# Kernel optimization log

Measured on AMD Instinct MI355X. Metric: run time of the kernel, lower is better.

The kernel has to match this reference:

```python
import jax, jax.numpy as jnp
import numpy as np

B, S, I, H, O = 4096, 512, 1, 16, 1


def setup_inputs() -> dict:
    key = jax.random.key(0)
    ks = jax.random.split(key, 7)
    bound = 1.0 / np.sqrt(H)
    return {
        "x": jax.random.normal(ks[0], (B, S, I), dtype=jnp.float32),
        "W_ih": jax.random.uniform(ks[1], (H, I), minval=-bound, maxval=bound, dtype=jnp.float32),
        "W_hh": jax.random.uniform(ks[2], (H, H), minval=-bound, maxval=bound, dtype=jnp.float32),
        "b_ih": jax.random.uniform(ks[3], (H,), minval=-bound, maxval=bound, dtype=jnp.float32),
        "b_hh": jax.random.uniform(ks[4], (H,), minval=-bound, maxval=bound, dtype=jnp.float32),
        "W_fc": jax.random.uniform(ks[5], (O, H), minval=-bound, maxval=bound, dtype=jnp.float32),
        "b_fc": jax.random.uniform(ks[6], (O,), minval=-bound, maxval=bound, dtype=jnp.float32),
    }


def reference(x, W_ih, W_hh, b_ih, b_hh, W_fc, b_fc):
    # Vanilla RNN (tanh): h_t = tanh(x_t W_ih^T + b_ih + h_{t-1} W_hh^T + b_hh)
    # Precompute input projections for all timesteps in one GEMM: [B,S,H]
    x_proj = jnp.einsum('bsi,hi->bsh', x, W_ih) + b_ih + b_hh

    def step(h, xp_t):  # h: [B,H], xp_t: [B,H]
        h_new = jnp.tanh(xp_t + h @ W_hh.T)
        return h_new, None

    h0 = jnp.zeros((x.shape[0], W_hh.shape[0]), dtype=x.dtype)
    h_last, _ = jax.lax.scan(step, h0, jnp.swapaxes(x_proj, 0, 1))  # scan over S
    # out[:, -1, :] -> final linear
    return h_last @ W_fc.T + b_fc
```

## Files before the change

### kernel.cpp

```cpp
#include <hip/hip_runtime.h>


#define S2LE 2.8853900817779268f

#define ROTI(v, N) __builtin_amdgcn_mov_dpp((v), 0x120 + (N), 0xF, 0xF, 0)
#define ROTF(v, N) __int_as_float(__builtin_amdgcn_mov_dpp(__float_as_int(v), 0x120 + (N), 0xF, 0xF, 0))

__global__ __launch_bounds__(64) void rnn_kernel(
    const float* __restrict__ x,
    const float* __restrict__ W_ih,
    const float* __restrict__ W_hh,
    const float* __restrict__ b_ih,
    const float* __restrict__ b_hh,
    const float* __restrict__ W_fc,
    const float* __restrict__ b_fc,
    float* __restrict__ out)
{
    const int li = (int)(threadIdx.x & 15u);
    const int b  = (int)((blockIdx.x * 64u + threadIdx.x) >> 4);

    const float* __restrict__ row = W_hh + li * 16;

    float w[16];
    w[0] = row[li] * S2LE;
#define LW(N) { int s_ = ROTI(li, N); w[N] = row[s_] * S2LE; }
    LW(1) LW(2) LW(3) LW(4) LW(5) LW(6) LW(7) LW(8)
    LW(9) LW(10) LW(11) LW(12) LW(13) LW(14) LW(15)
#undef LW

    const float wih  = W_ih[li] * S2LE;
    const float bias = (b_ih[li] + b_hh[li]) * S2LE;
    const float wfc  = W_fc[li];
    const float bfc  = b_fc[0];

    const float4* __restrict__ xv = (const float4*)(x + (size_t)b * 512);

    float h = 0.0f;
    float4 xc = xv[0];

#define STEP(XV) do { \
    float y0 = fmaf((XV), wih, bias); \
    y0 = fmaf(w[0], h, y0); \
    y0 = fmaf(w[1], ROTF(h, 1), y0); \
    y0 = fmaf(w[2], ROTF(h, 2), y0); \
    y0 = fmaf(w[3], ROTF(h, 3), y0); \
    float y1 = w[4] * ROTF(h, 4); \
    y1 = fmaf(w[5], ROTF(h, 5), y1); \
    y1 = fmaf(w[6], ROTF(h, 6), y1); \
    y1 = fmaf(w[7], ROTF(h, 7), y1); \
    float y2 = w[8] * ROTF(h, 8); \
    y2 = fmaf(w[9], ROTF(h, 9), y2); \
    y2 = fmaf(w[10], ROTF(h, 10), y2); \
    y2 = fmaf(w[11], ROTF(h, 11), y2); \
    float y3 = w[12] * ROTF(h, 12); \
    y3 = fmaf(w[13], ROTF(h, 13), y3); \
    y3 = fmaf(w[14], ROTF(h, 14), y3); \
    y3 = fmaf(w[15], ROTF(h, 15), y3); \
    y0 = (y0 + y1) + (y2 + y3); \
    float e_ = __builtin_amdgcn_exp2f(y0); \
    float r_ = __builtin_amdgcn_rcpf(e_ + 1.0f); \
    h = fmaf(-2.0f, r_, 1.0f); \
} while (0)

#pragma unroll 1
    for (int c = 0; c < 128; ++c) {
        float4 xn = xv[(c + 1) & 127];
        STEP(xc.x);
        STEP(xc.y);
        STEP(xc.z);
        STEP(xc.w);
        xc = xn;
    }
#undef STEP

    float p = h * wfc;
    p += ROTF(p, 8);
    p += ROTF(p, 4);
    p += ROTF(p, 2);
    p += ROTF(p, 1);
    if (li == 0) out[b] = p + bfc;
}

extern "C" void kernel_launch(void* const* d_in, const int* in_sizes, int n_in,
                              void* d_out, int out_size, void* d_ws, size_t ws_size,
                              hipStream_t stream) {
    const float* x    = (const float*)d_in[0];
    const float* W_ih = (const float*)d_in[1];
    const float* W_hh = (const float*)d_in[2];
    const float* b_ih = (const float*)d_in[3];
    const float* b_hh = (const float*)d_in[4];
    const float* W_fc = (const float*)d_in[5];
    const float* b_fc = (const float*)d_in[6];
    float* out = (float*)d_out;

    rnn_kernel<<<1024, 64, 0, stream>>>(x, W_ih, W_hh, b_ih, b_hh, W_fc, b_fc, out);
}
```

Before: 109.9 us.

## Compute RNN recurrence with fp16 MFMA on sigmoid-reparameterized hidden state

Replaces the per-lane DPP-rotate FMA chain with a 16x16x16 f16 MFMA per timestep. Each wave now handles 16 batch rows instead of 4, so the grid shrinks from 1024 to 256 blocks. The hidden state is rewritten as h = 1 - 2*sigmoid, with the row-sum of W_hh folded into the bias and -2 folded into the weights, which turns each step into one MFMA plus four exp/rcp per lane. The cost is fp16 precision for the weights and hidden state across 512 dependent steps, plus fewer waves to hide MFMA and transcendental latency.

```diff
diff --git a/kernel.cpp b/kernel.cpp
--- a/kernel.cpp
+++ b/kernel.cpp
@@ -3,8 +3,8 @@
 
 #define S2LE 2.8853900817779268f
 
-#define ROTI(v, N) __builtin_amdgcn_mov_dpp((v), 0x120 + (N), 0xF, 0xF, 0)
-#define ROTF(v, N) __int_as_float(__builtin_amdgcn_mov_dpp(__float_as_int(v), 0x120 + (N), 0xF, 0xF, 0))
+typedef _Float16 half4 __attribute__((ext_vector_type(4)));
+typedef float float4_ __attribute__((ext_vector_type(4)));
 
 __global__ __launch_bounds__(64) void rnn_kernel(
     const float* __restrict__ x,
@@ -16,69 +16,74 @@
     const float* __restrict__ b_fc,
     float* __restrict__ out)
 {
-    const int li = (int)(threadIdx.x & 15u);
-    const int b  = (int)((blockIdx.x * 64u + threadIdx.x) >> 4);
+    const int l  = (int)threadIdx.x;
+    const int n  = l & 15;
+    const int q  = l >> 4;
+    const int bb = (int)blockIdx.x * 16;
 
-    const float* __restrict__ row = W_hh + li * 16;
+    half4 afrag;
+#pragma unroll
+    for (int i = 0; i < 4; ++i)
+        afrag[i] = (_Float16)(-2.0f * S2LE * W_hh[n * 16 + (4 * q + i)]);
 
-    float w[16];
-    w[0] = row[li] * S2LE;
-#define LW(N) { int s_ = ROTI(li, N); w[N] = row[s_] * S2LE; }
-    LW(1) LW(2) LW(3) LW(4) LW(5) LW(6) LW(7) LW(8)
-    LW(9) LW(10) LW(11) LW(12) LW(13) LW(14) LW(15)
-#undef LW
+    float wih[4], bias[4], wfc[4];
+#pragma unroll
+    for (int r = 0; r < 4; ++r) {
+        int i = 4 * q + r;
+        float sw = 0.0f;
+#pragma unroll
+        for (int j = 0; j < 16; ++j) sw += W_hh[i * 16 + j];
+        wih[r]  = W_ih[i] * S2LE;
+        bias[r] = (b_ih[i] + b_hh[i] + sw) * S2LE;
+        wfc[r]  = W_fc[i];
+    }
 
-    const float wih  = W_ih[li] * S2LE;
-    const float bias = (b_ih[li] + b_hh[li]) * S2LE;
-    const float wfc  = W_fc[li];
-    const float bfc  = b_fc[0];
+    const float4_* __restrict__ xv =
+        (const float4_*)(x + (size_t)(bb + n) * 512);
 
-    const float4* __restrict__ xv = (const float4*)(x + (size_t)b * 512);
+    half4 bfrag;
+    bfrag[0] = bfrag[1] = bfrag[2] = bfrag[3] = (_Float16)0.5f;
+    float4_ gs;
 
-    float h = 0.0f;
-    float4 xc = xv[0];
+    float4_ xc = xv[0];
+    float4_ xn = xv[1];
 
-#define STEP(XV) do { \
-    float y0 = fmaf((XV), wih, bias); \
-    y0 = fmaf(w[0], h, y0); \
-    y0 = fmaf(w[1], ROTF(h, 1), y0); \
-    y0 = fmaf(w[2], ROTF(h, 2), y0); \
-    y0 = fmaf(w[3], ROTF(h, 3), y0); \
-    float y1 = w[4] * ROTF(h, 4); \
-    y1 = fmaf(w[5], ROTF(h, 5), y1); \
-    y1 = fmaf(w[6], ROTF(h, 6), y1); \
-    y1 = fmaf(w[7], ROTF(h, 7), y1); \
-    float y2 = w[8] * ROTF(h, 8); \
-    y2 = fmaf(w[9], ROTF(h, 9), y2); \
-    y2 = fmaf(w[10], ROTF(h, 10), y2); \
-    y2 = fmaf(w[11], ROTF(h, 11), y2); \
-    float y3 = w[12] * ROTF(h, 12); \
-    y3 = fmaf(w[13], ROTF(h, 13), y3); \
-    y3 = fmaf(w[14], ROTF(h, 14), y3); \
-    y3 = fmaf(w[15], ROTF(h, 15), y3); \
-    y0 = (y0 + y1) + (y2 + y3); \
-    float e_ = __builtin_amdgcn_exp2f(y0); \
-    float r_ = __builtin_amdgcn_rcpf(e_ + 1.0f); \
-    h = fmaf(-2.0f, r_, 1.0f); \
+#define STEP(XT) do { \
+    float4_ cc; \
+    cc[0] = fmaf((XT), wih[0], bias[0]); \
+    cc[1] = fmaf((XT), wih[1], bias[1]); \
+    cc[2] = fmaf((XT), wih[2], bias[2]); \
+    cc[3] = fmaf((XT), wih[3], bias[3]); \
+    float4_ y = __builtin_amdgcn_mfma_f32_16x16x16f16(afrag, bfrag, cc, 0, 0, 0); \
+    gs[0] = __builtin_amdgcn_rcpf(__builtin_amdgcn_exp2f(y[0]) + 1.0f); \
+    gs[1] = __builtin_amdgcn_rcpf(__builtin_amdgcn_exp2f(y[1]) + 1.0f); \
+    gs[2] = __builtin_amdgcn_rcpf(__builtin_amdgcn_exp2f(y[2]) + 1.0f); \
+    gs[3] = __builtin_amdgcn_rcpf(__builtin_amdgcn_exp2f(y[3]) + 1.0f); \
+    bfrag[0] = (_Float16)gs[0]; \
+    bfrag[1] = (_Float16)gs[1]; \
+    bfrag[2] = (_Float16)gs[2]; \
+    bfrag[3] = (_Float16)gs[3]; \
 } while (0)
 
 #pragma unroll 1
     for (int c = 0; c < 128; ++c) {
-        float4 xn = xv[(c + 1) & 127];
-        STEP(xc.x);
-        STEP(xc.y);
-        STEP(xc.z);
-        STEP(xc.w);
+        float4_ xf = xv[(c + 2) & 127];
+        STEP(xc[0]);
+        STEP(xc[1]);
+        STEP(xc[2]);
+        STEP(xc[3]);
         xc = xn;
+        xn = xf;
     }
 #undef STEP
 
-    float p = h * wfc;
-    p += ROTF(p, 8);
-    p += ROTF(p, 4);
-    p += ROTF(p, 2);
-    p += ROTF(p, 1);
-    if (li == 0) out[b] = p + bfc;
+    float p = 0.0f;
+#pragma unroll
+    for (int r = 0; r < 4; ++r)
+        p = fmaf(wfc[r], fmaf(-2.0f, gs[r], 1.0f), p);
+    p += __shfl_xor(p, 16, 64);
+    p += __shfl_xor(p, 32, 64);
+    if (q == 0) out[bb + n] = p + b_fc[0];
 }
 
 extern "C" void kernel_launch(void* const* d_in, const int* in_sizes, int n_in,
@@ -93,5 +98,5 @@
     const float* b_fc = (const float*)d_in[6];
     float* out = (float*)d_out;
 
-    rnn_kernel<<<1024, 64, 0, stream>>>(x, W_ih, W_hh, b_ih, b_hh, W_fc, b_fc, out);
+    rnn_kernel<<<256, 64, 0, stream>>>(x, W_ih, W_hh, b_ih, b_hh, W_fc, b_fc, out);
 }
```

Result: slower. 118.8 us (+8.2%).
